# Performance work log

Measured on AMD Instinct MI355X. Metric: run time of the kernel, lower is better.

The kernel has to match this reference:

```python
import jax, jax.numpy as jnp
import numpy as np

B, N, C = 2, 16384, 512
H, D = 8, 64            # heads, dim_head
QG = 64                 # n_global_queries
SC, CD = 256, 64        # context slices, context_dim


def _attn(q, k, v):
    # scaled_dot_product_attention with scale=1.0 (as in the module)
    s = jnp.einsum('bhqd,bhkd->bhqk', q, k)
    a = jax.nn.softmax(s, axis=-1)
    return jnp.einsum('bhqk,bhkd->bhqd', a, v)


def setup_inputs() -> dict:
    key = jax.random.key(0)
    ks = jax.random.split(key, 20)
    r = lambda i, shape, s=0.02: jax.random.normal(ks[i], shape, dtype=jnp.float32) * s
    return {
        'x': jax.random.normal(ks[0], (B, N, C), dtype=jnp.float32),
        'context': jax.random.normal(ks[1], (B, H, SC, CD), dtype=jnp.float32),
        'q_global': jax.random.normal(ks[2], (1, H, QG, D), dtype=jnp.float32),
        'Wp': r(3, (C, H * D)), 'bp': jnp.zeros((H * D,), jnp.float32),
        'Wk': r(4, (D, D)), 'bk': jnp.zeros((D,), jnp.float32),
        'Wv': r(5, (D, D)), 'bv': jnp.zeros((D,), jnp.float32),
        'Wcq': r(6, (D, D)), 'bcq': jnp.zeros((D,), jnp.float32),
        'Wck': r(7, (CD, D)), 'bck': jnp.zeros((D,), jnp.float32),
        'Wcv': r(8, (CD, D)), 'bcv': jnp.zeros((D,), jnp.float32),
        'state_mixing': jnp.zeros((), jnp.float32),
        'Wo': r(9, (H * D, C)), 'bo': jnp.zeros((C,), jnp.float32),
    }


def reference(x, context, q_global, Wp, bp, Wk, bk, Wv, bv,
              Wcq, bcq, Wck, bck, Wcv, bcv, state_mixing, Wo, bo):
    # input projection -> (B, H, N, D)
    x_mid = (x @ Wp + bp).reshape(B, N, H, D).transpose(0, 2, 1, 3)
    G = jnp.broadcast_to(q_global, (B, H, QG, D))
    k = x_mid @ Wk + bk                     # (B,H,N,D)
    v = x_mid @ Wv + bv
    # FLARE low-rank self-attention: tokens -> global queries -> tokens
    z = _attn(G, k, v)                      # (B,H,QG,D)
    self_attn = _attn(k, G, z)              # (B,H,N,D)
    # cross-attention to geometry context
    q = x_mid @ Wcq + bcq                   # (B,H,N,D)
    ck = context @ Wck + bck                # (B,H,SC,D)
    cv = context @ Wcv + bcv
    cross_attn = _attn(q, ck, cv)           # (B,H,N,D)
    # sigmoid-gated mix
    w = jax.nn.sigmoid(state_mixing)
    out = w * self_attn + (1.0 - w) * cross_attn
    out = out.transpose(0, 2, 1, 3).reshape(B, N, H * D)
    return out @ Wo + bo                    # (B,N,C); dropout=0 (eval)
```

## Files before the change

### kernel.cpp

```cpp
#include <hip/hip_runtime.h>

typedef __bf16 bf16;
typedef __bf16 bf16x8 __attribute__((ext_vector_type(8)));
typedef short short8 __attribute__((ext_vector_type(8)));
typedef float f32x4 __attribute__((ext_vector_type(4)));

__device__ __forceinline__ float ldf(const void* p, size_t i, int bf) {
  if (bf) {
    unsigned int u = ((const unsigned short*)p)[i];
    union { unsigned int ui; float f; } c;
    c.ui = u << 16;
    return c.f;
  }
  return ((const float*)p)[i];
}

__device__ __forceinline__ int sw8(int r) { return ((r ^ (r >> 2)) & 7) << 3; }
__device__ __forceinline__ int sw4(int r) { return ((r ^ (r >> 2)) & 3) << 3; }

__device__ __forceinline__ unsigned pk2(float a, float b) {
  union { bf16 h[2]; unsigned u; } c;
  c.h[0] = (bf16)a; c.h[1] = (bf16)b;
  return c.u;
}

__global__ void k_detect(const void* x, int* flag)
{
  int tid = threadIdx.x;
  int cnt = 0;
  for (int j = 0; j < 4; j++) {
    int i = (tid * 4 + j) * 2;
    unsigned int u = ((const unsigned short*)x)[i];
    union { unsigned int ui; float f; } c;
    c.ui = u << 16;
    float a = fabsf(c.f);
    if (a >= 1e-4f && a <= 100.f) cnt++;
  }
  for (int m = 1; m < 64; m <<= 1) cnt += __shfl_xor(cnt, m);
  if (tid == 0) *flag = (cnt > 128) ? 1 : 0;
}

__global__ __launch_bounds__(256)
void k_ctx(const int* flagp, const void* ctx, const void* Wck, const void* bck,
           const void* Wcv, const void* bcv, float* __restrict__ ck,
           float* __restrict__ cv)
{
  const int bf = *flagp;
  int rid = blockIdx.x * 4 + (threadIdx.x >> 6);
  int dp = threadIdx.x & 63;
  float a1 = 0.f, a2 = 0.f;
  for (int e = 0; e < 64; e++) {
    float c = ldf(ctx, (size_t)rid * 64 + e, bf);
    a1 += c * ldf(Wck, e * 64 + dp, bf);
    a2 += c * ldf(Wcv, e * 64 + dp, bf);
  }
  ck[rid * 64 + dp] = a1 + ldf(bck, dp, bf);
  cv[rid * 64 + dp] = a2 + ldf(bcv, dp, bf);
}

__global__ __launch_bounds__(256)
void k_fold(const int* flagp, const float* __restrict__ ck, const void* Wcq,
            const void* bcq, const void* qg, const void* Wk, const void* bk,
            float* __restrict__ ckq, float* __restrict__ cqb,
            float* __restrict__ Gk, float* __restrict__ gb)
{
  const int bf = *flagp;
  int bid = blockIdx.x, tid = threadIdx.x;
  if (bid < 1024) {
    int rid = bid * 4 + (tid >> 6), dp = tid & 63;
    const float* c = ck + (size_t)rid * 64;
    float a = 0.f;
    for (int o = 0; o < 64; o++) a += c[o] * ldf(Wcq, dp * 64 + o, bf);
    ckq[rid * 64 + dp] = a;
    if (dp == 0) {
      float s = 0.f;
      for (int o = 0; o < 64; o++) s += ldf(bcq, o, bf) * c[o];
      cqb[rid] = s;
    }
  } else {
    int i = (bid - 1024) * 256 + tid;
    int row = i >> 6, dIn = i & 63;
    float s = 0.f;
    for (int d = 0; d < 64; d++)
      s += ldf(qg, (size_t)row * 64 + d, bf) * ldf(Wk, dIn * 64 + d, bf);
    Gk[i] = s;
    if (dIn == 0) {
      float t = 0.f;
      for (int d = 0; d < 64; d++)
        t += ldf(qg, (size_t)row * 64 + d, bf) * ldf(bk, d, bf);
      gb[row] = t;
    }
  }
}

__global__ __launch_bounds__(256)
void k_prep(const float* __restrict__ ckq, const float* __restrict__ cv,
            const float* __restrict__ Gk, bf16* __restrict__ g_ckqb,
            bf16* __restrict__ g_cvtb, bf16* __restrict__ g_gkb)
{
  const int bid = blockIdx.x, tid = threadIdx.x;
  if (bid < 128) {
    const int bh = bid >> 3, chunk = bid & 7;
    const float* src = ckq + (size_t)bh * 16384;
    bf16* dst = g_ckqb + (size_t)bh * 16384;
    for (int e = tid; e < 2048; e += 256) {
      int idx = chunk * 2048 + e;
      int r = idx >> 6, c = idx & 63;
      dst[r * 64 + (c ^ sw8(r))] = (bf16)src[idx];
    }
  } else if (bid < 256) {
    const int t = bid - 128, bh = t >> 3, chunk = t & 7;
    const float* src = cv + (size_t)bh * 16384;
    bf16* dst = g_cvtb + (size_t)bh * 16384;
    for (int e = tid; e < 2048; e += 256) {
      int idx = chunk * 2048 + e;
      int d = idx >> 8, s = idx & 255;
      dst[d * 256 + (s ^ sw8(d))] = (bf16)src[s * 64 + d];
    }
  } else {
    const int half = bid - 256;
    for (int e = tid; e < 16384; e += 256) {
      int idx = half * 16384 + e;
      int hh = idx >> 12, r = (idx >> 6) & 63, c = idx & 63;
      g_gkb[hh * 4096 + r * 64 + (c ^ sw8(r))] = (bf16)Gk[idx];
    }
  }
}

__global__ __launch_bounds__(256)
void k_wtr(const int* flagp, const void* Wp, const void* Wo,
           bf16* __restrict__ WpT, bf16* __restrict__ WoT)
{
  const int bf = *flagp;
  const int bid = blockIdx.x, tid = threadIdx.x;
  const void* W = (bid < 64) ? Wp : Wo;
  bf16* WT = (bid < 64) ? WpT : WoT;
  const int tb = bid & 63, kb = tb & 7, nb = tb >> 3;
  __shared__ float t[64][65];
  for (int e = tid; e < 4096; e += 256) {
    int k = e >> 6, n = e & 63;
    t[k][n] = ldf(W, (size_t)(kb * 64 + k) * 512 + nb * 64 + n, bf);
  }
  __syncthreads();
  for (int e = tid; e < 4096; e += 256) {
    int n = e >> 6, k = e & 63;
    WT[(size_t)(nb * 64 + n) * 512 + kb * 64 + k] = (bf16)t[k][n];
  }
}

__global__ __launch_bounds__(256)
void k_gemm_mfma(const int* flagp, const void* A, const int amode,
                 const bf16* __restrict__ WT, const void* bias, void* out,
                 const int omode)
{
  __shared__ __attribute__((aligned(16))) bf16 AsB[2][128 * 32];
  __shared__ __attribute__((aligned(16))) bf16 BsB[2][128 * 32];

  const int bf = *flagp;
  const int abf = (amode == 1) || bf;
  const int tid = threadIdx.x;
  const int srow = tid >> 2, schk = tid & 3;

  const int orig = blockIdx.y * 4 + blockIdx.x;
  const int nid = (orig & 7) * 128 + (orig >> 3);
  const int m0 = (nid >> 2) * 128, n0 = (nid & 3) * 128;

  const int lane = tid & 63, wid = tid >> 6;
  const int lo = lane & 15, hi = lane >> 4;
  const int wm = (wid >> 1) * 64, wn = (wid & 1) * 64;

  f32x4 rf[2][2];
  bf16x8 rb[2];
  bf16x8 rw[2];

  auto ldreg = [&](int kt) {
    const int koff = kt * 32 + schk * 8;
#pragma unroll
    for (int p = 0; p < 2; p++) {
      const int row = p * 64 + srow;
      if (abf) {
        rb[p] = *(const bf16x8*)((const bf16*)A + (size_t)(m0 + row) * 512 + koff);
      } else {
        const float* ap = (const float*)A + (size_t)(m0 + row) * 512 + koff;
        rf[p][0] = *(const f32x4*)ap;
        rf[p][1] = *(const f32x4*)(ap + 4);
      }
      rw[p] = *(const bf16x8*)(WT + (size_t)(n0 + row) * 512 + koff);
    }
  };
  auto stlds = [&](bf16* As, bf16* Bs) {
    const int c = schk * 8;
#pragma unroll
    for (int p = 0; p < 2; p++) {
      const int row = p * 64 + srow;
      bf16x8 v;
      if (abf) {
        v = rb[p];
      } else {
#pragma unroll
        for (int j = 0; j < 4; j++) {
          v[j] = (bf16)rf[p][0][j];
          v[4 + j] = (bf16)rf[p][1][j];
        }
      }
      *(bf16x8*)&As[row * 32 + (c ^ sw4(row))] = v;
      *(bf16x8*)&Bs[row * 32 + (c ^ sw4(row))] = rw[p];
    }
  };

  f32x4 acc[4][4];
#pragma unroll
  for (int mt = 0; mt < 4; mt++)
#pragma unroll
    for (int nt = 0; nt < 4; nt++) acc[mt][nt] = f32x4{0.f, 0.f, 0.f, 0.f};

  ldreg(0);
  stlds(AsB[0], BsB[0]);
  __syncthreads();

  int cur = 0;
  for (int kt = 0; kt < 16; kt++) {
    if (kt < 15) ldreg(kt + 1);
    const bf16* Asc = AsB[cur];
    const bf16* Bsc = BsB[cur];
    short8 af[4], bq[4];
#pragma unroll
    for (int mt = 0; mt < 4; mt++) {
      int r = wm + mt * 16 + lo;
      af[mt] = *(const short8*)&Asc[r * 32 + ((hi * 8) ^ sw4(r))];
    }
#pragma unroll
    for (int nt = 0; nt < 4; nt++) {
      int r = wn + nt * 16 + lo;
      bq[nt] = *(const short8*)&Bsc[r * 32 + ((hi * 8) ^ sw4(r))];
    }
#pragma unroll
    for (int mt = 0; mt < 4; mt++)
#pragma unroll
      for (int nt = 0; nt < 4; nt++)
        acc[mt][nt] = __builtin_amdgcn_mfma_f32_16x16x32_bf16(
            af[mt], bq[nt], acc[mt][nt], 0, 0, 0);
    if (kt < 15) stlds(AsB[cur ^ 1], BsB[cur ^ 1]);
    __syncthreads();
    cur ^= 1;
  }

#pragma unroll
  for (int nt = 0; nt < 4; nt++) {
    const int col = n0 + wn + nt * 16 + lo;
    const float bj = ldf(bias, col, bf);
#pragma unroll
    for (int mt = 0; mt < 4; mt++)
#pragma unroll
      for (int r = 0; r < 4; r++) {
        const int rowg = m0 + wm + mt * 16 + hi * 4 + r;
        const float v = acc[mt][nt][r] + bj;
        const size_t oi = (size_t)rowg * 512 + col;
        if (omode == 0 || bf) ((bf16*)out)[oi] = (bf16)v;
        else                  ((float*)out)[oi] = v;
      }
  }
}

__global__ __launch_bounds__(256, 2)
void k_stageB(const float* __restrict__ Gk, const float* __restrict__ gb,
              const bf16* __restrict__ xm, float* __restrict__ zpart,
              float* __restrict__ lpart)
{
  __shared__ __attribute__((aligned(16))) char smem[8192 + 65536 + 1024];
  bf16* GkB = (bf16*)smem;
  const int tid = threadIdx.x;
  const int bh = blockIdx.y, b = bh >> 3, h = bh & 7;
  const int split = blockIdx.x;

#pragma unroll
  for (int it = 0; it < 2; it++) {
    int idx = tid + it * 256;
    int r = idx >> 3, c0 = (idx & 7) * 8;
    const float* g = Gk + (size_t)(h * 64 + r) * 64 + c0;
    bf16x8 v;
#pragma unroll
    for (int t = 0; t < 8; t++) v[t] = (bf16)g[t];
    *(bf16x8*)&GkB[r * 64 + (c0 ^ sw8(r))] = v;
  }
  __syncthreads();

  const int wid = tid >> 6, lane = tid & 63;
  const int lo = lane & 15, hi = lane >> 4;
  bf16*  Ew  = (bf16*)(smem + 8192 + wid * 16384);
  short* Xts = (short*)(smem + 8192 + wid * 16384 + 8192);

  short8 gk[4][2];
#pragma unroll
  for (int jt = 0; jt < 4; jt++)
#pragma unroll
    for (int ks = 0; ks < 2; ks++) {
      int r = jt * 16 + lo;
      gk[jt][ks] = *(const short8*)&GkB[r * 64 + ((ks * 32 + hi * 8) ^ sw8(r))];
    }
  float gbl[4][4];
#pragma unroll
  for (int jt = 0; jt < 4; jt++)
#pragma unroll
    for (int r = 0; r < 4; r++)
      gbl[jt][r] = gb[h * 64 + jt * 16 + hi * 4 + r];

  f32x4 zacc[4][4];
  float lacc[4][4];
#pragma unroll
  for (int jt = 0; jt < 4; jt++)
#pragma unroll
    for (int q = 0; q < 4; q++) {
      zacc[jt][q] = f32x4{0.f, 0.f, 0.f, 0.f};
      lacc[jt][q] = 0.f;
    }

  const int tokbase = split * 512 + wid * 128;
  for (int t = 0; t < 4; t++) {
    const int t0 = tokbase + t * 32;
    short8 bx[2][2];
#pragma unroll
    for (int tt = 0; tt < 2; tt++)
#pragma unroll
      for (int ks = 0; ks < 2; ks++)
        bx[tt][ks] = *(const short8*)(xm +
            (size_t)(b * 16384 + t0 + tt * 16 + lo) * 512 + h * 64 +
            ks * 32 + hi * 8);
#pragma unroll
    for (int tt = 0; tt < 2; tt++)
#pragma unroll
      for (int ks = 0; ks < 2; ks++)
#pragma unroll
        for (int e = 0; e < 8; e++) {
          int d = ks * 32 + hi * 8 + e;
          int tok = tt * 16 + lo;
          Xts[d * 64 + (tok ^ sw8(d))] = bx[tt][ks][e];
        }
    f32x4 s[4][2];
#pragma unroll
    for (int jt = 0; jt < 4; jt++)
#pragma unroll
      for (int tt = 0; tt < 2; tt++) s[jt][tt] = f32x4{0.f, 0.f, 0.f, 0.f};
#pragma unroll
    for (int ks = 0; ks < 2; ks++)
#pragma unroll
      for (int jt = 0; jt < 4; jt++)
#pragma unroll
        for (int tt = 0; tt < 2; tt++)
          s[jt][tt] = __builtin_amdgcn_mfma_f32_16x16x32_bf16(
              gk[jt][ks], bx[tt][ks], s[jt][tt], 0, 0, 0);
#pragma unroll
    for (int jt = 0; jt < 4; jt++)
#pragma unroll
      for (int tt = 0; tt < 2; tt++)
#pragma unroll
        for (int r = 0; r < 4; r++) {
          int j = jt * 16 + hi * 4 + r;
          int tok = tt * 16 + lo;
          float e = __expf(s[jt][tt][r] + gbl[jt][r]);
          lacc[jt][r] += e;
          Ew[j * 64 + (tok ^ sw8(j))] = (bf16)e;
        }
    short8 ea[4], xb[4];
#pragma unroll
    for (int jt = 0; jt < 4; jt++) {
      int r = jt * 16 + lo;
      ea[jt] = *(const short8*)&Ew[r * 64 + ((hi * 8) ^ sw8(r))];
    }
#pragma unroll
    for (int dt = 0; dt < 4; dt++) {
      int d = dt * 16 + lo;
      xb[dt] = *(const short8*)(Xts + d * 64 + ((hi * 8) ^ sw8(d)));
    }
#pragma unroll
    for (int jt = 0; jt < 4; jt++)
#pragma unroll
      for (int dt = 0; dt < 4; dt++)
        zacc[jt][dt] = __builtin_amdgcn_mfma_f32_16x16x32_bf16(
            ea[jt], xb[dt], zacc[jt][dt], 0, 0, 0);
  }

  float* lred = (float*)(smem + 8192 + 65536);
#pragma unroll
  for (int jt = 0; jt < 4; jt++)
#pragma unroll
    for (int r = 0; r < 4; r++) {
      float v = lacc[jt][r];
      for (int m = 1; m < 16; m <<= 1) v += __shfl_xor(v, m);
      if (lo == 0) lred[wid * 64 + jt * 16 + hi * 4 + r] = v;
    }
  __syncthreads();

  float* zred = (float*)(smem + 8192);
#pragma unroll
  for (int jt = 0; jt < 4; jt++)
#pragma unroll
    for (int dt = 0; dt < 4; dt++)
#pragma unroll
      for (int r = 0; r < 4; r++)
        zred[wid * 4096 + (jt * 16 + hi * 4 + r) * 64 + dt * 16 + lo] =
            zacc[jt][dt][r];
  __syncthreads();

  const size_t pbase = ((size_t)bh * 32 + split) * 4096;
  for (int i = tid; i < 4096; i += 256)
    zpart[pbase + i] =
        zred[i] + zred[4096 + i] + zred[8192 + i] + zred[12288 + i];
  if (tid < 64)
    lpart[((size_t)bh * 32 + split) * 64 + tid] =
        lred[tid] + lred[64 + tid] + lred[128 + tid] + lred[192 + tid];
}

__global__ __launch_bounds__(256)
void k_zred(const float* __restrict__ zpart, const float* __restrict__ lpart,
            float* __restrict__ zsum, float* __restrict__ lsumG)
{
  const int bh = blockIdx.y, chunk = blockIdx.x;
  const int i = chunk * 256 + threadIdx.x;
  float s = 0.f;
  for (int sp = 0; sp < 32; sp++)
    s += zpart[((size_t)bh * 32 + sp) * 4096 + i];
  zsum[(size_t)bh * 4096 + i] = s;
  if (chunk == 0 && threadIdx.x < 64) {
    float t = 0.f;
    for (int sp = 0; sp < 32; sp++)
      t += lpart[((size_t)bh * 32 + sp) * 64 + threadIdx.x];
    lsumG[bh * 64 + threadIdx.x] = t;
  }
}

__global__ __launch_bounds__(64)
void k_znorm2(const int* flagp, const float* __restrict__ zsum,
              const float* __restrict__ lsumG, const void* Wv, const void* bv,
              bf16* __restrict__ g_ztb)
{
  const int bf = *flagp;
  const int j = blockIdx.x, bh = blockIdx.y, d = threadIdx.x;
  __shared__ float zl[64];
  zl[d] = zsum[(size_t)bh * 4096 + j * 64 + d];
  __syncthreads();
  const float inv = 1.f / lsumG[bh * 64 + j];
  float s = 0.f;
#pragma unroll 8
  for (int e = 0; e < 64; e++) s += zl[e] * ldf(Wv, e * 64 + d, bf);
  g_ztb[(size_t)bh * 4096 + d * 64 + (j ^ sw8(d))] =
      (bf16)(s * inv + ldf(bv, d, bf));
}

template <int NCH, int VSTR, int NB>
__device__ __forceinline__ void attn_part2(
    const bf16* __restrict__ Aq, const bf16* __restrict__ BvT,
    const float (&breg)[NB], const short8 (&ax)[2][2],
    int lo, int hi, f32x4 (&accO)[2][4], float (&ltok)[2])
{
#pragma unroll
  for (int ch = 0; ch < NCH; ch++) {
    const int c0 = ch * 32;
    f32x4 s[2][2];
#pragma unroll
    for (int ct = 0; ct < 2; ct++)
#pragma unroll
      for (int rt = 0; rt < 2; rt++) s[ct][rt] = f32x4{0.f, 0.f, 0.f, 0.f};
#pragma unroll
    for (int ks = 0; ks < 2; ks++) {
      short8 aq[2];
#pragma unroll
      for (int ct = 0; ct < 2; ct++) {
        int n = c0 + ct * 16 + lo;
        aq[ct] = *(const short8*)(Aq + n * 64 + ((ks * 32 + hi * 8) ^ sw8(n)));
      }
#pragma unroll
      for (int ct = 0; ct < 2; ct++)
#pragma unroll
        for (int rt = 0; rt < 2; rt++)
          s[ct][rt] = __builtin_amdgcn_mfma_f32_16x16x32_bf16(
              aq[ct], ax[rt][ks], s[ct][rt], 0, 0, 0);
    }
    unsigned w[2][2][2];
#pragma unroll
    for (int ct = 0; ct < 2; ct++) {
      float b[4];
#pragma unroll
      for (int r = 0; r < 4; r++)
        b[r] = __shfl(breg[(c0 + ct * 16) >> 6],
                      ((c0 + ct * 16) & 63) + hi * 4 + r);
#pragma unroll
      for (int rt = 0; rt < 2; rt++) {
        float e0 = __expf(s[ct][rt][0] + b[0]);
        float e1 = __expf(s[ct][rt][1] + b[1]);
        float e2 = __expf(s[ct][rt][2] + b[2]);
        float e3 = __expf(s[ct][rt][3] + b[3]);
        ltok[rt] += e0 + e1 + e2 + e3;
        w[rt][ct][0] = pk2(e0, e1);
        w[rt][ct][1] = pk2(e2, e3);
      }
    }
#pragma unroll
    for (int rt = 0; rt < 2; rt++) {
      const int s0 = lo + 32 * (hi & 1);
      unsigned t00 = __shfl(w[rt][0][0], s0);
      unsigned t10 = __shfl(w[rt][1][0], s0);
      unsigned t01 = __shfl(w[rt][0][1], s0);
      unsigned t11 = __shfl(w[rt][1][1], s0);
      unsigned t20 = __shfl(w[rt][0][0], s0 + 16);
      unsigned t30 = __shfl(w[rt][1][0], s0 + 16);
      unsigned t21 = __shfl(w[rt][0][1], s0 + 16);
      unsigned t31 = __shfl(w[rt][1][1], s0 + 16);
      union { unsigned u[4]; short8 s8; } pa;
      const bool c1 = (hi >> 1) != 0;
      pa.u[0] = c1 ? t10 : t00;
      pa.u[1] = c1 ? t11 : t01;
      pa.u[2] = c1 ? t30 : t20;
      pa.u[3] = c1 ? t31 : t21;
#pragma unroll
      for (int dt = 0; dt < 4; dt++) {
        int d = dt * 16 + lo;
        short8 bv = *(const short8*)(BvT + d * VSTR + ((c0 + hi * 8) ^ sw8(d)));
        accO[rt][dt] = __builtin_amdgcn_mfma_f32_16x16x32_bf16(
            pa.s8, bv, accO[rt][dt], 0, 0, 0);
      }
    }
  }
}

__global__ __launch_bounds__(512, 4)
void k_attn(const int* flagp, const bf16* __restrict__ g_gkb,
            const bf16* __restrict__ g_ztb, const bf16* __restrict__ g_ckqb,
            const bf16* __restrict__ g_cvtb, const float* __restrict__ cqb,
            const float* __restrict__ gb, const bf16* __restrict__ xm,
            const void* smix, bf16* __restrict__ selfmid)
{
  __shared__ __attribute__((aligned(16))) bf16 S[40960];
  bf16* GkB  = S;
  bf16* zTB  = S + 4096;
  bf16* ckqB = S + 8192;
  bf16* cvTB = S + 24576;

  const int tid = threadIdx.x;
  const int bh = blockIdx.y, b = bh >> 3, h = bh & 7;
  const int lane = tid & 63;

  {
    int i = tid;
    *(bf16x8*)&GkB[i * 8] = *(const bf16x8*)&g_gkb[(size_t)h * 4096 + i * 8];
    *(bf16x8*)&zTB[i * 8] = *(const bf16x8*)&g_ztb[(size_t)bh * 4096 + i * 8];
#pragma unroll
    for (int it = 0; it < 4; it++) {
      int j = tid + it * 512;
      *(bf16x8*)&ckqB[j * 8] =
          *(const bf16x8*)&g_ckqb[(size_t)bh * 16384 + j * 8];
      *(bf16x8*)&cvTB[j * 8] =
          *(const bf16x8*)&g_cvtb[(size_t)bh * 16384 + j * 8];
    }
  }
  float creg[4], greg[1];
#pragma unroll
  for (int q = 0; q < 4; q++) creg[q] = cqb[bh * 256 + q * 64 + lane];
  greg[0] = gb[h * 64 + lane];
  __syncthreads();

  const int wid = tid >> 6;
  const int lo = lane & 15, hi = lane >> 4;
  const int m0 = blockIdx.x * 256 + wid * 32;

  short8 ax[2][2];
#pragma unroll
  for (int rt = 0; rt < 2; rt++)
#pragma unroll
    for (int ks = 0; ks < 2; ks++)
      ax[rt][ks] = *(const short8*)(xm +
          (size_t)(b * 16384 + m0 + rt * 16 + lo) * 512 + h * 64 +
          ks * 32 + hi * 8);

  f32x4 accS[2][4], accC[2][4];
  float l1[2] = {0.f, 0.f}, l2[2] = {0.f, 0.f};
#pragma unroll
  for (int rt = 0; rt < 2; rt++)
#pragma unroll
    for (int dt = 0; dt < 4; dt++) {
      accS[rt][dt] = f32x4{0.f, 0.f, 0.f, 0.f};
      accC[rt][dt] = f32x4{0.f, 0.f, 0.f, 0.f};
    }

  attn_part2<2, 64, 1>(GkB, zTB, greg, ax, lo, hi, accS, l1);
  attn_part2<8, 256, 4>(ckqB, cvTB, creg, ax, lo, hi, accC, l2);

#pragma unroll
  for (int rt = 0; rt < 2; rt++) {
    float a = l1[rt], c = l2[rt];
    a += __shfl_xor(a, 16); a += __shfl_xor(a, 32);
    c += __shfl_xor(c, 16); c += __shfl_xor(c, 32);
    l1[rt] = 1.f / a;
    l2[rt] = 1.f / c;
  }

  const int bf = *flagp;
  const float wmix = 1.f / (1.f + __expf(-ldf(smix, 0, bf)));
#pragma unroll
  for (int rt = 0; rt < 2; rt++)
#pragma unroll
    for (int r = 0; r < 4; r++) {
      const float invS = __shfl(l1[rt], hi * 4 + r);
      const float invC = __shfl(l2[rt], hi * 4 + r);
      int row = m0 + rt * 16 + hi * 4 + r;
      size_t off = (size_t)(b * 16384 + row) * 512 + h * 64;
#pragma unroll
      for (int dt = 0; dt < 4; dt++) {
        float vS = accS[rt][dt][r] * invS;
        float vC = accC[rt][dt][r] * invC;
        selfmid[off + dt * 16 + lo] = (bf16)(wmix * vS + (1.f - wmix) * vC);
      }
    }
}

extern "C" void kernel_launch(void* const* d_in, const int* in_sizes, int n_in,
                              void* d_out, int out_size, void* d_ws, size_t ws_size,
                              hipStream_t stream)
{
  const void* x    = d_in[0];
  const void* ctx  = d_in[1];
  const void* qg   = d_in[2];
  const void* Wp   = d_in[3];  const void* bp  = d_in[4];
  const void* Wk   = d_in[5];  const void* bk  = d_in[6];
  const void* Wv   = d_in[7];  const void* bv  = d_in[8];
  const void* Wcq  = d_in[9];  const void* bcq = d_in[10];
  const void* Wck  = d_in[11]; const void* bck = d_in[12];
  const void* Wcv  = d_in[13]; const void* bcv = d_in[14];
  const void* smix = d_in[15];
  const void* Wo   = d_in[16]; const void* bo  = d_in[17];

  char* ws = (char*)d_ws;
  int*   flag    = (int*)(ws);
  float* ck      = (float*)(ws + 256);
  float* cv      = (float*)(ws + 1048832);
  float* ckq     = (float*)(ws + 2097408);
  float* cqb     = (float*)(ws + 3145984);
  float* Gk      = (float*)(ws + 3162368);
  float* gb      = (float*)(ws + 3293440);
  bf16*  g_cvtb  = (bf16*)(ws + 3295744);
  bf16*  g_ckqb  = (bf16*)(ws + 3820032);
  bf16*  g_gkb   = (bf16*)(ws + 4348160);
  bf16*  g_ztb   = (bf16*)(ws + 4413696);
  bf16*  xm      = (bf16*)(ws + 5396736);
  bf16*  selfmid = (bf16*)(ws + 38951168);
  bf16*  WpT     = (bf16*)(ws + 256);
  bf16*  WoT     = (bf16*)(ws + 256 + 524288);
  float* zpart   = (float*)(ws + 38951168);
  float* lpart   = (float*)(ws + 38951168 + 8388608);
  float* zsum    = (float*)(ws + 38951168 + 8519680);
  float* lsumG   = (float*)(ws + 38951168 + 8781824);

  k_detect<<<1, 64, 0, stream>>>(x, flag);

  k_ctx<<<1024, 256, 0, stream>>>(flag, ctx, Wck, bck, Wcv, bcv, ck, cv);
  k_fold<<<1152, 256, 0, stream>>>(flag, ck, Wcq, bcq, qg, Wk, bk,
                                   ckq, cqb, Gk, gb);

  k_prep<<<258, 256, 0, stream>>>(ckq, cv, Gk, g_ckqb, g_cvtb, g_gkb);
  k_wtr<<<128, 256, 0, stream>>>(flag, Wp, Wo, WpT, WoT);

  k_gemm_mfma<<<dim3(4, 256), 256, 0, stream>>>(flag, x, 0, WpT, bp, xm, 0);

  k_stageB<<<dim3(32, 16), 256, 0, stream>>>(Gk, gb, xm, zpart, lpart);
  k_zred<<<dim3(16, 16), 256, 0, stream>>>(zpart, lpart, zsum, lsumG);
  k_znorm2<<<dim3(64, 16), 64, 0, stream>>>(flag, zsum, lsumG, Wv, bv, g_ztb);

  k_attn<<<dim3(64, 16), 512, 0, stream>>>(flag, g_gkb, g_ztb, g_ckqb, g_cvtb,
                                           cqb, (const float*)gb, xm, smix,
                                           selfmid);

  k_gemm_mfma<<<dim3(4, 256), 256, 0, stream>>>(flag, selfmid, 1, WoT, bo,
                                                d_out, 1);
}
```

Measured before the change: 380.3 us.

## Deepen GEMM register prefetch to two stages and pad LDS rows instead of swizzle

The MFMA GEMM now keeps two register staging sets, issuing global loads two k-tiles ahead so each load has more time to land before its shared-memory store. The XOR swizzle on shared tiles is replaced by padding rows from 32 to 40 elements, which simplifies address math. The cost is more registers per thread, which may lower occupancy, and a little more shared memory.

```diff
diff --git a/kernel.cpp b/kernel.cpp
--- a/kernel.cpp
+++ b/kernel.cpp
@@ -16,7 +16,6 @@
 }
 
 __device__ __forceinline__ int sw8(int r) { return ((r ^ (r >> 2)) & 7) << 3; }
-__device__ __forceinline__ int sw4(int r) { return ((r ^ (r >> 2)) & 3) << 3; }
 
 __device__ __forceinline__ unsigned pk2(float a, float b) {
   union { bf16 h[2]; unsigned u; } c;
@@ -153,8 +152,8 @@
                  const bf16* __restrict__ WT, const void* bias, void* out,
                  const int omode)
 {
-  __shared__ __attribute__((aligned(16))) bf16 AsB[2][128 * 32];
-  __shared__ __attribute__((aligned(16))) bf16 BsB[2][128 * 32];
+  __shared__ __attribute__((aligned(16))) bf16 AsB[2][128 * 40];
+  __shared__ __attribute__((aligned(16))) bf16 BsB[2][128 * 40];
 
   const int bf = *flagp;
   const int abf = (amode == 1) || bf;
@@ -169,42 +168,43 @@
   const int lo = lane & 15, hi = lane >> 4;
   const int wm = (wid >> 1) * 64, wn = (wid & 1) * 64;
 
-  f32x4 rf[2][2];
-  bf16x8 rb[2];
-  bf16x8 rw[2];
-
-  auto ldreg = [&](int kt) {
+  f32x4 rf[2][2][2];
+  bf16x8 rb[2][2];
+  bf16x8 rw[2][2];
+
+  auto ldreg = [&](int sel, int kt) {
     const int koff = kt * 32 + schk * 8;
 #pragma unroll
     for (int p = 0; p < 2; p++) {
       const int row = p * 64 + srow;
       if (abf) {
-        rb[p] = *(const bf16x8*)((const bf16*)A + (size_t)(m0 + row) * 512 + koff);
+        rb[sel][p] =
+            *(const bf16x8*)((const bf16*)A + (size_t)(m0 + row) * 512 + koff);
       } else {
         const float* ap = (const float*)A + (size_t)(m0 + row) * 512 + koff;
-        rf[p][0] = *(const f32x4*)ap;
-        rf[p][1] = *(const f32x4*)(ap + 4);
+        rf[sel][p][0] = *(const f32x4*)ap;
+        rf[sel][p][1] = *(const f32x4*)(ap + 4);
       }
-      rw[p] = *(const bf16x8*)(WT + (size_t)(n0 + row) * 512 + koff);
+      rw[sel][p] = *(const bf16x8*)(WT + (size_t)(n0 + row) * 512 + koff);
     }
   };
-  auto stlds = [&](bf16* As, bf16* Bs) {
+  auto stlds = [&](int sel, bf16* As, bf16* Bs) {
     const int c = schk * 8;
 #pragma unroll
     for (int p = 0; p < 2; p++) {
       const int row = p * 64 + srow;
       bf16x8 v;
       if (abf) {
-        v = rb[p];
+        v = rb[sel][p];
       } else {
 #pragma unroll
         for (int j = 0; j < 4; j++) {
-          v[j] = (bf16)rf[p][0][j];
-          v[4 + j] = (bf16)rf[p][1][j];
+          v[j] = (bf16)rf[sel][p][0][j];
+          v[4 + j] = (bf16)rf[sel][p][1][j];
         }
       }
-      *(bf16x8*)&As[row * 32 + (c ^ sw4(row))] = v;
-      *(bf16x8*)&Bs[row * 32 + (c ^ sw4(row))] = rw[p];
+      *(bf16x8*)&As[row * 40 + c] = v;
+      *(bf16x8*)&Bs[row * 40 + c] = rw[sel][p];
     }
   };
 
@@ -214,33 +214,30 @@
 #pragma unroll
     for (int nt = 0; nt < 4; nt++) acc[mt][nt] = f32x4{0.f, 0.f, 0.f, 0.f};
 
-  ldreg(0);
-  stlds(AsB[0], BsB[0]);
+  ldreg(0, 0);
+  stlds(0, AsB[0], BsB[0]);
+  ldreg(0, 1);
   __syncthreads();
 
   int cur = 0;
   for (int kt = 0; kt < 16; kt++) {
-    if (kt < 15) ldreg(kt + 1);
+    if (kt < 14) ldreg((kt + 1) & 1, kt + 2);
     const bf16* Asc = AsB[cur];
     const bf16* Bsc = BsB[cur];
     short8 af[4], bq[4];
 #pragma unroll
-    for (int mt = 0; mt < 4; mt++) {
-      int r = wm + mt * 16 + lo;
-      af[mt] = *(const short8*)&Asc[r * 32 + ((hi * 8) ^ sw4(r))];
-    }
-#pragma unroll
-    for (int nt = 0; nt < 4; nt++) {
-      int r = wn + nt * 16 + lo;
-      bq[nt] = *(const short8*)&Bsc[r * 32 + ((hi * 8) ^ sw4(r))];
-    }
+    for (int mt = 0; mt < 4; mt++)
+      af[mt] = *(const short8*)&Asc[(wm + mt * 16 + lo) * 40 + hi * 8];
+#pragma unroll
+    for (int nt = 0; nt < 4; nt++)
+      bq[nt] = *(const short8*)&Bsc[(wn + nt * 16 + lo) * 40 + hi * 8];
 #pragma unroll
     for (int mt = 0; mt < 4; mt++)
 #pragma unroll
       for (int nt = 0; nt < 4; nt++)
         acc[mt][nt] = __builtin_amdgcn_mfma_f32_16x16x32_bf16(
             af[mt], bq[nt], acc[mt][nt], 0, 0, 0);
-    if (kt < 15) stlds(AsB[cur ^ 1], BsB[cur ^ 1]);
+    if (kt < 15) stlds(kt & 1, AsB[cur ^ 1], BsB[cur ^ 1]);
     __syncthreads();
     cur ^= 1;
   }
```

Result: no change. 380.3 us (-0.0%).
